# Optimization experiments

Hardware: AMD Instinct MI355X
Metric: run time of the kernel (lower is better)

## Reference

```python
import jax, jax.numpy as jnp
import numpy as np

N, T, D, H, NH, BS = 4, 4096, 512, 8, 4, 64
DH = D // H                 # head dim = 64
NB = T // BS                # n_buckets = 64
CS = NH * NB                # chunk_size = 256
L = NH * T                  # sorted sequence length per head


def setup_inputs() -> dict:
    key = jax.random.key(0)
    ks = jax.random.split(key, 4)
    x = jax.random.normal(ks[0], (N, T, D), jnp.float32)
    W_Q = jax.random.normal(ks[1], (D, D), jnp.float32) * (D ** -0.5)
    W_V = jax.random.normal(ks[2], (D, D), jnp.float32) * (D ** -0.5)
    b_Q = jnp.zeros((D,), jnp.float32)
    b_V = jnp.zeros((D,), jnp.float32)
    gamma = jnp.ones((D,), jnp.float32)
    beta = jnp.zeros((D,), jnp.float32)
    # per-head random rotations: (dim_head, num_hashes, n_buckets // 2)
    rotations = jax.random.normal(ks[3], (H, DH, NH, NB // 2), jnp.float32)
    return {"x": x, "W_Q": W_Q, "b_Q": b_Q, "W_V": W_V, "b_V": b_V,
            "gamma": gamma, "beta": beta, "rotations": rotations}


def _look_one_back(a):
    # concat each chunk with the previous chunk (wrap-around for chunk 0)
    extra = jnp.concatenate([a[:, -1:], a[:, :-1]], axis=1)
    return jnp.concatenate([a, extra], axis=2)


def _lsh_head(qk, v, rot):
    # qk, v: [N, T, DH]; rot: [DH, NH, NB//2]
    rotated = jnp.einsum('btf,fhi->bhti', qk, rot)               # [N,NH,T,NB//2]
    rotated = jnp.concatenate([rotated, -rotated], axis=-1)       # [N,NH,T,NB]
    buckets = jnp.argmax(rotated, axis=-1)                        # [N,NH,T]
    offsets = (jnp.arange(NH) * NB)[None, :, None]
    buckets = (buckets + offsets).reshape(N, L)                   # [N, NH*T]

    ticker = jnp.broadcast_to(jnp.arange(L)[None, :], (N, L))
    buckets_and_t = T * buckets + (ticker % T)                    # unique keys
    sticker = jnp.argsort(buckets_and_t, axis=-1)                 # sorted ticker ids
    undo_sort = jnp.argsort(sticker, axis=-1)
    st = sticker % T                                              # original positions

    sqk = jnp.take_along_axis(qk, st[..., None], axis=1)          # [N,L,DH]
    sv = jnp.take_along_axis(v, st[..., None], axis=1)

    bq_t = st.reshape(N, CS, -1)                                  # [N,CS,BS]
    bqk = sqk.reshape(N, CS, -1, DH)
    bv = sv.reshape(N, CS, -1, DH)
    bq = bqk
    bk = bqk / (jnp.linalg.norm(bqk, axis=-1, keepdims=True) + 1e-6)

    bk = _look_one_back(bk)                                       # [N,CS,2*BS,DH]
    bv = _look_one_back(bv)
    bkv_t = _look_one_back(bq_t)

    dots = jnp.einsum('bcie,bcje->bcij', bq, bk) * (DH ** -0.5)   # [N,CS,BS,2BS]

    # mask out pairs hashed to different buckets
    q_sb = jnp.take_along_axis(buckets, sticker, axis=1).reshape(N, CS, -1)
    kv_sb = _look_one_back(q_sb)
    dots = jnp.where(q_sb[:, :, :, None] != kv_sb[:, :, None, :], -1e9, dots)
    # down-weight self-attention (same position)
    dots = jnp.where(bq_t[:, :, :, None] == bkv_t[:, :, None, :], -1e-5, dots)

    lse = jax.nn.logsumexp(dots, axis=-1, keepdims=True)
    probs = jnp.exp(dots - lse)
    bo = jnp.einsum('bcij,bcje->bcie', probs, bv)                 # [N,CS,BS,DH]

    so = bo.reshape(N, L, DH)
    slog = lse.reshape(N, L)
    o = jnp.take_along_axis(so, undo_sort[..., None], axis=1)
    logits = jnp.take_along_axis(slog, undo_sort, axis=1)

    o = o.reshape(N, NH, T, DH)
    logits = logits.reshape(N, NH, T, 1)
    pw = jnp.exp(logits - jax.nn.logsumexp(logits, axis=1, keepdims=True))
    return jnp.sum(o * pw, axis=1)                                # [N,T,DH]


def reference(x, W_Q, b_Q, W_V, b_V, gamma, beta, rotations):
    Q = x @ W_Q + b_Q
    V = x @ W_V + b_V
    Qh = Q.reshape(N, T, H, DH).transpose(2, 0, 1, 3)             # [H,N,T,DH]
    Vh = V.reshape(N, T, H, DH).transpose(2, 0, 1, 3)
    outs = jax.vmap(_lsh_head)(Qh, Vh, rotations)                 # [H,N,T,DH]
    out = outs.transpose(1, 2, 0, 3).reshape(N, T, D)
    mu = out.mean(axis=-1, keepdims=True)
    var = out.var(axis=-1, keepdims=True)
    return gamma * (out - mu) / jnp.sqrt(var + 1e-3) + beta
```

## Files before the change

kernel.cpp:

```cpp
#include <hip/hip_runtime.h>
#include <hip/hip_bf16.h>

#define N_ 4
#define T_ 4096
#define D_ 512
#define H_ 8
#define DH_ 64
#define NH_ 4
#define NB_ 64
#define CS_ 256
#define L_ 16384

typedef unsigned short u16;
typedef unsigned int u32;
typedef __attribute__((ext_vector_type(8))) short short8;
typedef __attribute__((ext_vector_type(8))) _Float16 half8;
typedef __attribute__((ext_vector_type(4))) float f32x4;
typedef __attribute__((ext_vector_type(2))) float f32x2;

__device__ __forceinline__ u16 f2bf(float x){
    union { float f; u32 u; } c; c.f = x;
    u32 u = c.u;
    u32 r = (u + 0x7FFFu + ((u >> 16) & 1u)) >> 16;
    return (u16)r;
}
__device__ __forceinline__ float bf2f(u16 b){
    union { u32 u; float f; } c; c.u = ((u32)b) << 16;
    return c.f;
}
__device__ __forceinline__ u16 f2h(float x){
    _Float16 h = (_Float16)x;
    u16 r; __builtin_memcpy(&r, &h, 2); return r;
}

#define PK_LO(acc, a, b) \
    asm("v_pk_fma_f32 %0, %1, %2, %0 op_sel:[0,0,0] op_sel_hi:[0,1,1]" \
        : "+v"(acc) : "v"(a), "v"(b))
#define PK_HI(acc, a, b) \
    asm("v_pk_fma_f32 %0, %1, %2, %0 op_sel:[1,0,0] op_sel_hi:[1,1,1]" \
        : "+v"(acc) : "v"(a), "v"(b))

#define VSWZ(d) ((((d) >> 3) ^ ((d) & 7)))

__global__ __launch_bounds__(256) void k_decWv(const float* __restrict__ Wv,
        u16* __restrict__ wvt){
    __shared__ float tile[32][33];
    const int tid = threadIdx.x;
    const int kt = blockIdx.x * 32, nt = blockIdx.y * 32;
    const int tx = tid & 31, ty = tid >> 5;
    #pragma unroll
    for (int i = 0; i < 4; ++i)
        tile[ty + i * 8][tx] = Wv[(size_t)(kt + ty + i * 8) * 512 + nt + tx];
    __syncthreads();
    #pragma unroll
    for (int i = 0; i < 4; ++i){
        int n = ty + i * 8;
        wvt[(size_t)(nt + n) * 512 + kt + tx] = f2h(tile[tx][n]);
    }
}

__global__ __launch_bounds__(512, 4) void k_qv(const float* __restrict__ x,
        const float* __restrict__ Wq, const float* __restrict__ bq,
        const u16* __restrict__ wvt, const float* __restrict__ bv,
        float* __restrict__ Q, u16* __restrict__ Qbf, float* __restrict__ qinv,
        u16* __restrict__ Vbf){
    __shared__ __align__(16) char uLDS[33792];

    const int bid = blockIdx.x;
    const int role = (bid >> 8) & 1;
    const int id = ((bid >> 9) << 8) | (bid & 255);
    const int mb = (id & 127) * 128;
    const int nbi = id >> 7;
    const int nb = nbi * 128;
    const int tid = threadIdx.x;

    if (role == 0){
        typedef float (*pan_t)[16][132];
        pan_t sA = (pan_t)uLDS;
        pan_t sB = (pan_t)(uLDS + 16896);
        const int tx = tid & 31, ty = tid >> 5;
        f32x2 acc2[8][2];
        #pragma unroll
        for (int i = 0; i < 8; ++i){
            acc2[i][0] = (f32x2){0.f, 0.f};
            acc2[i][1] = (f32x2){0.f, 0.f};
        }
        const int mA = tid >> 2, kA = (tid & 3) * 4;
        const int kB = tid >> 5, cB = (tid & 31) * 4;
        const float* xp = &x[(size_t)(mb + mA) * 512 + kA];
        const float* wp = &Wq[(size_t)kB * 512 + nb + cB];
        float4 pa = *(const float4*)xp;
        float4 pb = *(const float4*)wp;

        for (int k0 = 0; k0 < 512; k0 += 16){
            const int p = (k0 >> 4) & 1;
            sA[p][kA + 0][mA] = pa.x; sA[p][kA + 1][mA] = pa.y;
            sA[p][kA + 2][mA] = pa.z; sA[p][kA + 3][mA] = pa.w;
            *(float4*)&sB[p][kB][cB] = pb;
            __syncthreads();
            if (k0 < 496){
                pa = *(const float4*)(xp + k0 + 16);
                pb = *(const float4*)(wp + (size_t)(k0 + 16) * 512);
            }
            #pragma unroll
            for (int kk = 0; kk < 16; ++kk){
                float4 va0 = *(const float4*)&sA[p][kk][ty * 8];
                float4 va1 = *(const float4*)&sA[p][kk][ty * 8 + 4];
                float4 vb  = *(const float4*)&sB[p][kk][tx * 4];
                f32x2 a2[4], b2[2];
                a2[0] = (f32x2){va0.x, va0.y}; a2[1] = (f32x2){va0.z, va0.w};
                a2[2] = (f32x2){va1.x, va1.y}; a2[3] = (f32x2){va1.z, va1.w};
                b2[0] = (f32x2){vb.x, vb.y};   b2[1] = (f32x2){vb.z, vb.w};
                #pragma unroll
                for (int i = 0; i < 8; ++i){
                    if (i & 1){
                        PK_HI(acc2[i][0], a2[i >> 1], b2[0]);
                        PK_HI(acc2[i][1], a2[i >> 1], b2[1]);
                    } else {
                        PK_LO(acc2[i][0], a2[i >> 1], b2[0]);
                        PK_LO(acc2[i][1], a2[i >> 1], b2[1]);
                    }
                }
            }
        }

        float4 vbq = *(const float4*)&bq[nb + tx * 4];
        const int h = nbi * 2 + (tx >> 4);
        const int d0 = (tx & 15) * 4;
        #pragma unroll
        for (int i = 0; i < 8; ++i){
            float o0 = acc2[i][0].x + vbq.x;
            float o1 = acc2[i][0].y + vbq.y;
            float o2 = acc2[i][1].x + vbq.z;
            float o3 = acc2[i][1].y + vbq.w;
            int m = mb + ty * 8 + i;
            int n = m >> 12, t = m & (T_ - 1);
            float4 q4; q4.x = o0; q4.y = o1; q4.z = o2; q4.w = o3;
            *(float4*)&Q[(size_t)m * 512 + nb + tx * 4] = q4;
            float ss = o0 * o0 + o1 * o1 + o2 * o2 + o3 * o3;
            #pragma unroll
            for (int s = 8; s >= 1; s >>= 1) ss += __shfl_xor(ss, s, 64);
            size_t rowb = (size_t)(h * N_ + n) * T_ + t;
            if ((tx & 15) == 0) qinv[rowb] = 1.f / (sqrtf(ss) + 1e-6f);
            ushort4 qb4;
            qb4.x = f2bf(o0); qb4.y = f2bf(o1); qb4.z = f2bf(o2); qb4.w = f2bf(o3);
            *(ushort4*)&Qbf[rowb * 64 + d0] = qb4;
        }
    } else {
        if (tid >= 256) return;
        u16* sA = (u16*)uLDS;
        u16* sB = (u16*)(uLDS + 10240);
        const int w = tid >> 6, lane = tid & 63;
        const int quad = lane >> 4, cc = lane & 15;
        const int wm = (w & 1) * 64, wn = (w >> 1) * 64;
        f32x4 acc[4][4];
        #pragma unroll
        for (int i = 0; i < 4; ++i)
            #pragma unroll
            for (int j = 0; j < 4; ++j) acc[i][j] = (f32x4){0.f, 0.f, 0.f, 0.f};

        for (int k0 = 0; k0 < 512; k0 += 32){
            #pragma unroll
            for (int i = 0; i < 2; ++i){
                int idx = i * 256 + tid;
                int m = idx >> 2, ks = idx & 3;
                const float* xs = &x[(size_t)(mb + m) * 512 + k0 + ks * 8];
                float4 f0 = *(const float4*)xs;
                float4 f1 = *(const float4*)(xs + 4);
                short8 s;
                s[0] = (short)f2h(f0.x); s[1] = (short)f2h(f0.y);
                s[2] = (short)f2h(f0.z); s[3] = (short)f2h(f0.w);
                s[4] = (short)f2h(f1.x); s[5] = (short)f2h(f1.y);
                s[6] = (short)f2h(f1.z); s[7] = (short)f2h(f1.w);
                *(short8*)&sA[m * 40 + ks * 8] = s;
                *(short8*)&sB[m * 40 + ks * 8] =
                    *(const short8*)&wvt[(size_t)(nb + m) * 512 + k0 + ks * 8];
            }
            __syncthreads();
            half8 a[4], b[4];
            #pragma unroll
            for (int i = 0; i < 4; ++i){
                a[i] = *(const half8*)&sA[(wm + i * 16 + cc) * 40 + quad * 8];
                b[i] = *(const half8*)&sB[(wn + i * 16 + cc) * 40 + quad * 8];
            }
            #pragma unroll
            for (int i = 0; i < 4; ++i)
                #pragma unroll
                for (int j = 0; j < 4; ++j)
                    acc[i][j] = __builtin_amdgcn_mfma_f32_16x16x32_f16(a[i], b[j], acc[i][j], 0, 0, 0);
            __syncthreads();
        }
        #pragma unroll
        for (int i = 0; i < 4; ++i)
            #pragma unroll
            for (int j = 0; j < 4; ++j){
                int c = nb + wn + j * 16 + cc;
                int hh = c >> 6, d = c & 63;
                float bi = bv[c];
                #pragma unroll
                for (int r = 0; r < 4; ++r){
                    int m = mb + wm + i * 16 + quad * 4 + r;
                    int n = m >> 12, t = m & (T_ - 1);
                    Vbf[((size_t)(hh * N_ + n) * T_ + t) * 64 + d] = f2bf(acc[i][j][r] + bi);
                }
            }
    }
}

__global__ __launch_bounds__(256) void k_rot(const float* __restrict__ Q,
        const float* __restrict__ rot, int* __restrict__ buckets){
    const int tb = blockIdx.x * 32;
    const int n = blockIdx.y, h = blockIdx.z;
    const int hn = h * N_ + n;
    __shared__ float Rs[64 * 128];
    __shared__ float Qs[32][64];
    const int tid = threadIdx.x;
    const float* rh = rot + (size_t)h * (64 * 128);
    for (int idx = tid; idx < 8192; idx += 256){
        int f = idx >> 7, rem = idx & 127, jj = rem >> 5, i2 = rem & 31;
        Rs[f * 128 + i2 * 4 + jj] = rh[idx];
    }
    for (int i = tid; i < 2048; i += 256){
        int t = i >> 6, f = i & 63;
        Qs[t][f] = Q[(size_t)(n * T_ + tb + t) * 512 + h * 64 + f];
    }
    __syncthreads();
    const int tx = tid & 31, tg = tid >> 5;
    f32x2 r2[4][2];
    #pragma unroll
    for (int tt = 0; tt < 4; ++tt){
        r2[tt][0] = (f32x2){0.f, 0.f};
        r2[tt][1] = (f32x2){0.f, 0.f};
    }
    for (int f = 0; f < 64; f += 2){
        f32x2 qf[4];
        #pragma unroll
        for (int tt = 0; tt < 4; ++tt)
            qf[tt] = *(const f32x2*)&Qs[tg * 4 + tt][f];
        float4 rv0 = *(const float4*)&Rs[f * 128 + tx * 4];
        float4 rv1 = *(const float4*)&Rs[(f + 1) * 128 + tx * 4];
        f32x2 b0[2], b1[2];
        b0[0] = (f32x2){rv0.x, rv0.y}; b0[1] = (f32x2){rv0.z, rv0.w};
        b1[0] = (f32x2){rv1.x, rv1.y}; b1[1] = (f32x2){rv1.z, rv1.w};
        #pragma unroll
        for (int tt = 0; tt < 4; ++tt){
            PK_LO(r2[tt][0], qf[tt], b0[0]);
            PK_LO(r2[tt][1], qf[tt], b0[1]);
            PK_HI(r2[tt][0], qf[tt], b1[0]);
            PK_HI(r2[tt][1], qf[tt], b1[1]);
        }
    }
    #pragma unroll
    for (int tt = 0; tt < 4; ++tt){
        #pragma unroll
        for (int jj = 0; jj < 4; ++jj){
            float rval = (jj < 2) ? r2[tt][0][jj] : r2[tt][1][jj - 2];
            float bv = rval; int bi = tx;
            float nv = -bv;
            if (nv > bv){ bv = nv; bi = 32 + tx; }
            #pragma unroll
            for (int m = 16; m >= 1; m >>= 1){
                float ov = __shfl_xor(bv, m, 32);
                int   oi = __shfl_xor(bi, m, 32);
                if (ov > bv || (ov == bv && oi < bi)){ bv = ov; bi = oi; }
            }
            if (tx == 0){
                int t = tb + tg * 4 + tt;
                buckets[(size_t)hn * L_ + jj * T_ + t] = bi + jj * 64;
            }
        }
    }
}

__global__ __launch_bounds__(256) void k_hist(const int* __restrict__ buckets,
        int* __restrict__ hist){
    const int tile = blockIdx.x, hn = blockIdx.y;
    const int tid = threadIdx.x;
    __shared__ int h[256];
    h[tid] = 0;
    __syncthreads();
    int b = buckets[(size_t)hn * L_ + tile * 256 + tid];
    atomicAdd(&h[b], 1);
    __syncthreads();
    hist[((size_t)hn * 64 + tile) * 256 + tid] = h[tid];
}

__global__ __launch_bounds__(256) void k_scan(int* __restrict__ hist,
        int* __restrict__ bucketStart){
    const int hn = blockIdx.x;
    const int b = threadIdx.x;
    int* hh = hist + (size_t)hn * 64 * 256;
    int run = 0;
    for (int tl = 0; tl < 64; ++tl){
        int v = hh[tl * 256 + b];
        hh[tl * 256 + b] = run;
        run += v;
    }
    __shared__ int s[256];
    s[b] = run;
    __syncthreads();
    for (int off = 1; off < 256; off <<= 1){
        int add = (b >= off) ? s[b - off] : 0;
        __syncthreads();
        s[b] += add;
        __syncthreads();
    }
    bucketStart[hn * 256 + b] = s[b] - run;
}

__global__ __launch_bounds__(256) void k_scatter(const int* __restrict__ buckets,
        const int* __restrict__ offs, const int* __restrict__ bucketStart,
        int* __restrict__ sticker){
    const int tile = blockIdx.x, hn = blockIdx.y;
    const int tid = threadIdx.x;
    __shared__ int sb[256];
    const int i = tile * 256 + tid;
    const int b = buckets[(size_t)hn * L_ + i];
    sb[tid] = b;
    __syncthreads();
    int rank = 0;
    #pragma unroll 8
    for (int j = 0; j < 256; ++j){
        int v = sb[j];
        rank += (j < tid && v == b) ? 1 : 0;
    }
    int pos = bucketStart[hn * 256 + b]
            + offs[((size_t)hn * 64 + tile) * 256 + b]
            + rank;
    sticker[(size_t)hn * L_ + pos] = i;
}

__global__ __launch_bounds__(256) void k_attn(const u16* __restrict__ Qbf,
        const u16* __restrict__ Vbf, const float* __restrict__ qinv,
        const int* __restrict__ buckets, const int* __restrict__ sticker,
        u16* __restrict__ o_hash, float* __restrict__ logit_hash){
    const int blk_c = blockIdx.x, n = blockIdx.y, h = blockIdx.z;
    const int hn = h * N_ + n;
    const int tid = threadIdx.x;
    const int w = tid >> 6, lane = tid & 63;
    const int quad = lane >> 4, cc = lane & 15;

    __shared__ __align__(16) u16 sQP[128 * 64];
    __shared__ __align__(16) u16 sVt[64 * 128];
    __shared__ int s_idx[128], s_buck[128], s_t[128];
    __shared__ float s_inv[128];
    __shared__ float s_lse[64];
    u16* const sQ = sQP;
    u16* const sP = sQP;

    if (tid < 128){
        int cprev = (blk_c + CS_ - 1) & (CS_ - 1);
        int pos = (tid < 64) ? blk_c * 64 + tid : cprev * 64 + (tid - 64);
        int idx = sticker[(size_t)hn * L_ + pos];
        s_idx[tid] = idx;
        s_buck[tid] = buckets[(size_t)hn * L_ + idx];
        int t = idx & (T_ - 1);
        s_t[tid] = t;
        s_inv[tid] = qinv[(size_t)hn * T_ + t] * 0.125f;
    }
    __syncthreads();

    const int r0 = tid >> 3, l8 = tid & 7;
    #pragma unroll
    for (int it = 0; it < 4; ++it){
        int r = it * 32 + r0;
        size_t gb = ((size_t)hn * T_ + s_t[r]) * 64 + l8 * 8;
        short8 qv = *(const short8*)&Qbf[gb];
        *(short8*)&sQ[r * 64 + ((l8 ^ (r & 7)) * 8)] = qv;
        short8 vv = *(const short8*)&Vbf[gb];
        #pragma unroll
        for (int i = 0; i < 8; ++i){
            int d = l8 * 8 + i;
            sVt[d * 128 + (((r >> 3) ^ VSWZ(d)) * 8) + (r & 7)] = (u16)vv[i];
        }
    }
    __syncthreads();

    f32x4 dacc[8];
    #pragma unroll
    for (int j = 0; j < 8; ++j) dacc[j] = (f32x4){0.f, 0.f, 0.f, 0.f};
    const int qrow = w * 16 + cc;
    #pragma unroll
    for (int kc = 0; kc < 2; ++kc){
        short8 afrag = *(const short8*)&sQ[qrow * 64 + (((kc * 4 + quad) ^ (cc & 7)) * 8)];
        #pragma unroll
        for (int kt = 0; kt < 8; ++kt){
            int krow = kt * 16 + cc;
            short8 bfrag = *(const short8*)&sQ[krow * 64 + (((kc * 4 + quad) ^ (cc & 7)) * 8)];
            dacc[kt] = __builtin_amdgcn_mfma_f32_16x16x32_bf16(afrag, bfrag, dacc[kt], 0, 0, 0);
        }
    }

    int bq[4], tq[4];
    #pragma unroll
    for (int r = 0; r < 4; ++r){
        int q = w * 16 + quad * 4 + r;
        bq[r] = s_buck[q]; tq[r] = s_t[q];
    }
    float mrow[4] = {-1e30f, -1e30f, -1e30f, -1e30f};
    #pragma unroll
    for (int kt = 0; kt < 8; ++kt){
        int kk = kt * 16 + cc;
        float inv = s_inv[kk];
        int bk = s_buck[kk], tk = s_t[kk];
        #pragma unroll
        for (int r = 0; r < 4; ++r){
            float d = dacc[kt][r] * inv;
            if (bk != bq[r]) d = -1e9f;
            if (tk == tq[r]) d = -1e-5f;
            dacc[kt][r] = d;
            mrow[r] = fmaxf(mrow[r], d);
        }
    }
    #pragma unroll
    for (int r = 0; r < 4; ++r)
        #pragma unroll
        for (int m = 8; m >= 1; m >>= 1)
            mrow[r] = fmaxf(mrow[r], __shfl_xor(mrow[r], m, 64));
    float srow[4] = {0.f, 0.f, 0.f, 0.f};
    #pragma unroll
    for (int kt = 0; kt < 8; ++kt)
        #pragma unroll
        for (int r = 0; r < 4; ++r){
            float e = __expf(dacc[kt][r] - mrow[r]);
            dacc[kt][r] = e;
            srow[r] += e;
        }
    #pragma unroll
    for (int r = 0; r < 4; ++r)
        #pragma unroll
        for (int m = 8; m >= 1; m >>= 1)
            srow[r] += __shfl_xor(srow[r], m, 64);
    float lse[4], pscale[4];
    #pragma unroll
    for (int r = 0; r < 4; ++r){
        lse[r] = mrow[r] + __logf(srow[r]);
        pscale[r] = 1.f / srow[r];
    }
    if (cc == 0){
        #pragma unroll
        for (int r = 0; r < 4; ++r) s_lse[w * 16 + quad * 4 + r] = lse[r];
    }

    __syncthreads();

    #pragma unroll
    for (int kt = 0; kt < 8; ++kt){
        int kk = kt * 16 + cc;
        #pragma unroll
        for (int r = 0; r < 4; ++r){
            int q = w * 16 + quad * 4 + r;
            sP[q * 128 + (((kk >> 3) ^ (q & 15)) * 8) + (kk & 7)] =
                f2bf(dacc[kt][r] * pscale[r]);
        }
    }
    __syncthreads();

    f32x4 oacc[4];
    #pragma unroll
    for (int j = 0; j < 4; ++j) oacc[j] = (f32x4){0.f, 0.f, 0.f, 0.f};
    #pragma unroll
    for (int kc = 0; kc < 4; ++kc){
        short8 afrag = *(const short8*)&sP[qrow * 128 + (((kc * 4 + quad) ^ cc) * 8)];
        #pragma unroll
        for (int nt = 0; nt < 4; ++nt){
            int d = nt * 16 + cc;
            short8 bfrag = *(const short8*)&sVt[d * 128 + (((kc * 4 + quad) ^ VSWZ(d)) * 8)];
            oacc[nt] = __builtin_amdgcn_mfma_f32_16x16x32_bf16(afrag, bfrag, oacc[nt], 0, 0, 0);
        }
    }

    #pragma unroll
    for (int r = 0; r < 4; ++r){
        int q = w * 16 + quad * 4 + r;
        int si = s_idx[q];
        int jj = si >> 12; int t = si & (T_ - 1);
        size_t base = ((size_t)(hn * NH_ + jj) * T_ + t) * 64;
        #pragma unroll
        for (int nt = 0; nt < 4; ++nt)
            o_hash[base + nt * 16 + cc] = f2bf(oacc[nt][r]);
    }
    if (tid < 64){
        int si = s_idx[tid]; int jj = si >> 12; int t = si & (T_ - 1);
        logit_hash[(size_t)(hn * NH_ + jj) * T_ + t] = s_lse[tid];
    }
}

__global__ __launch_bounds__(256) void k_comb(const u16* __restrict__ o_hash,
        const float* __restrict__ logit_hash, const float* __restrict__ gamma,
        const float* __restrict__ beta, float* __restrict__ out){
    const int t = blockIdx.x, n = blockIdx.y;
    const int tid = threadIdx.x;
    __shared__ float s_pw[32];
    __shared__ float s_x[512];
    __shared__ float s_red[8];
    __shared__ float s_mu, s_rs;
    if (tid < 32){
        int h = tid >> 2, j = tid & 3;
        s_pw[tid] = logit_hash[(size_t)((h * N_ + n) * NH_ + j) * T_ + t];
    }
    __syncthreads();
    if (tid < 8){
        int h = tid;
        float m = -1e30f;
        #pragma unroll
        for (int j = 0; j < 4; ++j) m = fmaxf(m, s_pw[h * 4 + j]);
        float l = 0.f;
        #pragma unroll
        for (int j = 0; j < 4; ++j) l += __expf(s_pw[h * 4 + j] - m);
        float ls = m + __logf(l);
        #pragma unroll
        for (int j = 0; j < 4; ++j) s_pw[h * 4 + j] = __expf(s_pw[h * 4 + j] - ls);
    }
    __syncthreads();
    float va[2];
    #pragma unroll
    for (int i = 0; i < 2; ++i){
        int cidx = tid + i * 256;
        int h = cidx >> 6, d = cidx & 63;
        size_t base = (size_t)((h * N_ + n) * NH_) * T_ * 64;
        float acc = 0.f;
        #pragma unroll
        for (int j = 0; j < 4; ++j)
            acc += s_pw[h * 4 + j] * bf2f(o_hash[base + ((size_t)j * T_ + t) * 64 + d]);
        s_x[cidx] = acc; va[i] = acc;
    }
    float s1 = va[0] + va[1];
    float s2 = va[0] * va[0] + va[1] * va[1];
    #pragma unroll
    for (int m = 32; m >= 1; m >>= 1){
        s1 += __shfl_xor(s1, m, 64);
        s2 += __shfl_xor(s2, m, 64);
    }
    const int lane = tid & 63, w = tid >> 6;
    if (lane == 0){ s_red[w] = s1; s_red[4 + w] = s2; }
    __syncthreads();
    if (tid == 0){
        float S1 = s_red[0] + s_red[1] + s_red[2] + s_red[3];
        float S2 = s_red[4] + s_red[5] + s_red[6] + s_red[7];
        float mu = S1 / 512.f;
        float var = S2 / 512.f - mu * mu;
        s_mu = mu; s_rs = 1.f / sqrtf(var + 1e-3f);
    }
    __syncthreads();
    #pragma unroll
    for (int i = 0; i < 2; ++i){
        int cidx = tid + i * 256;
        out[((size_t)(n * T_ + t)) * 512 + cidx] =
            gamma[cidx] * (s_x[cidx] - s_mu) * s_rs + beta[cidx];
    }
}

extern "C" void kernel_launch(void* const* d_in, const int* in_sizes, int n_in,
                              void* d_out, int out_size, void* d_ws, size_t ws_size,
                              hipStream_t stream){
    const float* x     = (const float*)d_in[0];
    const float* Wq    = (const float*)d_in[1];
    const float* bq    = (const float*)d_in[2];
    const float* Wv    = (const float*)d_in[3];
    const float* bv    = (const float*)d_in[4];
    const float* gamma = (const float*)d_in[5];
    const float* beta  = (const float*)d_in[6];
    const float* rot   = (const float*)d_in[7];
    char* ws = (char*)d_ws;
    float* Q        = (float*)(ws + 0);
    u16*   o_hash   = (u16*)  (ws + 0);
    u16*   Qbf      = (u16*)  (ws + 67108864);
    u16*   Vbf      = (u16*)  (ws + 83886080);
    float* qinv     = (float*)(ws + 100663296);
    int*   buckets  = (int*)  (ws + 101187584);
    int*   sticker  = (int*)  (ws + 103284736);
    float* logit    = (float*)(ws + 105381888);
    int*   hist     = (int*)  (ws + 107479040);
    int*   bstart   = (int*)  (ws + 109576192);
    u16*   wvt      = (u16*)  (ws + 109608960);

    hipLaunchKernelGGL(k_decWv,   dim3(16, 16),     dim3(256), 0, stream,
                       Wv, wvt);
    hipLaunchKernelGGL(k_qv,      dim3(1024),       dim3(512), 0, stream,
                       x, Wq, bq, wvt, bv, Q, Qbf, qinv, Vbf);
    hipLaunchKernelGGL(k_rot,     dim3(128, 4, 8),  dim3(256), 0, stream,
                       Q, rot, buckets);
    hipLaunchKernelGGL(k_hist,    dim3(64, 32),     dim3(256), 0, stream,
                       buckets, hist);
    hipLaunchKernelGGL(k_scan,    dim3(32),         dim3(256), 0, stream,
                       hist, bstart);
    hipLaunchKernelGGL(k_scatter, dim3(64, 32),     dim3(256), 0, stream,
                       buckets, hist, bstart, sticker);
    hipLaunchKernelGGL(k_attn,    dim3(256, 4, 8),  dim3(256), 0, stream,
                       Qbf, Vbf, qinv, buckets, sticker, o_hash, logit);
    hipLaunchKernelGGL(k_comb,    dim3(4096, 4),    dim3(256), 0, stream,
                       o_hash, logit, gamma, beta, (float*)d_out);
}
```

Baseline: 380.7 us.

## Interleave hash outputs per token, warp-per-token combine, amortize rotation loads, MFMA priority

Four changes land together. The o_hash and logit_hash layouts are reordered so the four hash rounds of each token sit next to each other, and k_comb now gives each wavefront one token, doing the softmax over rounds and the layer norm with shuffles instead of shared memory and block barriers. k_rot handles 64 tokens per block instead of 32, so each rotation-matrix load into LDS serves twice as many tokens, at the cost of fewer blocks. The attention MFMA loops are wrapped in s_setprio to raise wave priority while issuing matrix ops.

Result: slower. 397.5 us (+4.4%).

```diff
diff --git a/kernel.cpp b/kernel.cpp
--- a/kernel.cpp
+++ b/kernel.cpp
@@ -209,64 +209,66 @@
 
 __global__ __launch_bounds__(256) void k_rot(const float* __restrict__ Q,
         const float* __restrict__ rot, int* __restrict__ buckets){
-    const int tb = blockIdx.x * 32;
+    const int tb = blockIdx.x * 64;
     const int n = blockIdx.y, h = blockIdx.z;
     const int hn = h * N_ + n;
     __shared__ float Rs[64 * 128];
-    __shared__ float Qs[32][64];
+    __shared__ float Qs[64][64];
     const int tid = threadIdx.x;
     const float* rh = rot + (size_t)h * (64 * 128);
     for (int idx = tid; idx < 8192; idx += 256){
         int f = idx >> 7, rem = idx & 127, jj = rem >> 5, i2 = rem & 31;
         Rs[f * 128 + i2 * 4 + jj] = rh[idx];
     }
-    for (int i = tid; i < 2048; i += 256){
+    for (int i = tid; i < 4096; i += 256){
         int t = i >> 6, f = i & 63;
         Qs[t][f] = Q[(size_t)(n * T_ + tb + t) * 512 + h * 64 + f];
     }
     __syncthreads();
     const int tx = tid & 31, tg = tid >> 5;
-    f32x2 r2[4][2];
-    #pragma unroll
-    for (int tt = 0; tt < 4; ++tt){
-        r2[tt][0] = (f32x2){0.f, 0.f};
-        r2[tt][1] = (f32x2){0.f, 0.f};
-    }
-    for (int f = 0; f < 64; f += 2){
-        f32x2 qf[4];
-        #pragma unroll
-        for (int tt = 0; tt < 4; ++tt)
-            qf[tt] = *(const f32x2*)&Qs[tg * 4 + tt][f];
-        float4 rv0 = *(const float4*)&Rs[f * 128 + tx * 4];
-        float4 rv1 = *(const float4*)&Rs[(f + 1) * 128 + tx * 4];
-        f32x2 b0[2], b1[2];
-        b0[0] = (f32x2){rv0.x, rv0.y}; b0[1] = (f32x2){rv0.z, rv0.w};
-        b1[0] = (f32x2){rv1.x, rv1.y}; b1[1] = (f32x2){rv1.z, rv1.w};
+    for (int half = 0; half < 2; ++half){
+        f32x2 r2[4][2];
         #pragma unroll
         for (int tt = 0; tt < 4; ++tt){
-            PK_LO(r2[tt][0], qf[tt], b0[0]);
-            PK_LO(r2[tt][1], qf[tt], b0[1]);
-            PK_HI(r2[tt][0], qf[tt], b1[0]);
-            PK_HI(r2[tt][1], qf[tt], b1[1]);
-        }
-    }
-    #pragma unroll
-    for (int tt = 0; tt < 4; ++tt){
-        #pragma unroll
-        for (int jj = 0; jj < 4; ++jj){
-            float rval = (jj < 2) ? r2[tt][0][jj] : r2[tt][1][jj - 2];
-            float bv = rval; int bi = tx;
-            float nv = -bv;
-            if (nv > bv){ bv = nv; bi = 32 + tx; }
-            #pragma unroll
-            for (int m = 16; m >= 1; m >>= 1){
-                float ov = __shfl_xor(bv, m, 32);
-                int   oi = __shfl_xor(bi, m, 32);
-                if (ov > bv || (ov == bv && oi < bi)){ bv = ov; bi = oi; }
-            }
-            if (tx == 0){
-                int t = tb + tg * 4 + tt;
-                buckets[(size_t)hn * L_ + jj * T_ + t] = bi + jj * 64;
+            r2[tt][0] = (f32x2){0.f, 0.f};
+            r2[tt][1] = (f32x2){0.f, 0.f};
+        }
+        for (int f = 0; f < 64; f += 2){
+            f32x2 qf[4];
+            #pragma unroll
+            for (int tt = 0; tt < 4; ++tt)
+                qf[tt] = *(const f32x2*)&Qs[half * 32 + tg * 4 + tt][f];
+            float4 rv0 = *(const float4*)&Rs[f * 128 + tx * 4];
+            float4 rv1 = *(const float4*)&Rs[(f + 1) * 128 + tx * 4];
+            f32x2 b0[2], b1[2];
+            b0[0] = (f32x2){rv0.x, rv0.y}; b0[1] = (f32x2){rv0.z, rv0.w};
+            b1[0] = (f32x2){rv1.x, rv1.y}; b1[1] = (f32x2){rv1.z, rv1.w};
+            #pragma unroll
+            for (int tt = 0; tt < 4; ++tt){
+                PK_LO(r2[tt][0], qf[tt], b0[0]);
+                PK_LO(r2[tt][1], qf[tt], b0[1]);
+                PK_HI(r2[tt][0], qf[tt], b1[0]);
+                PK_HI(r2[tt][1], qf[tt], b1[1]);
+            }
+        }
+        #pragma unroll
+        for (int tt = 0; tt < 4; ++tt){
+            #pragma unroll
+            for (int jj = 0; jj < 4; ++jj){
+                float rval = (jj < 2) ? r2[tt][0][jj] : r2[tt][1][jj - 2];
+                float bv = rval; int bi = tx;
+                float nv = -bv;
+                if (nv > bv){ bv = nv; bi = 32 + tx; }
+                #pragma unroll
+                for (int m = 16; m >= 1; m >>= 1){
+                    float ov = __shfl_xor(bv, m, 32);
+                    int   oi = __shfl_xor(bi, m, 32);
+                    if (ov > bv || (ov == bv && oi < bi)){ bv = ov; bi = oi; }
+                }
+                if (tx == 0){
+                    int t = tb + half * 32 + tg * 4 + tt;
+                    buckets[(size_t)hn * L_ + jj * T_ + t] = bi + jj * 64;
+                }
             }
         }
     }
@@ -380,6 +382,7 @@
     #pragma unroll
     for (int j = 0; j < 8; ++j) dacc[j] = (f32x4){0.f, 0.f, 0.f, 0.f};
     const int qrow = w * 16 + cc;
+    __builtin_amdgcn_s_setprio(1);
     #pragma unroll
     for (int kc = 0; kc < 2; ++kc){
         short8 afrag = *(const short8*)&sQ[qrow * 64 + (((kc * 4 + quad) ^ (cc & 7)) * 8)];
@@ -390,6 +393,7 @@
             dacc[kt] = __builtin_amdgcn_mfma_f32_16x16x32_bf16(afrag, bfrag, dacc[kt], 0, 0, 0);
         }
     }
+    __builtin_amdgcn_s_setprio(0);
 
     int bq[4], tq[4];
     #pragma unroll
@@ -459,6 +463,7 @@
     f32x4 oacc[4];
     #pragma unroll
     for (int j = 0; j < 4; ++j) oacc[j] = (f32x4){0.f, 0.f, 0.f, 0.f};
+    __builtin_amdgcn_s_setprio(1);
     #pragma unroll
     for (int kc = 0; kc < 4; ++kc){
         short8 afrag = *(const short8*)&sP[qrow * 128 + (((kc * 4 + quad) ^ cc) * 8)];
@@ -469,85 +474,72 @@
             oacc[nt] = __builtin_amdgcn_mfma_f32_16x16x32_bf16(afrag, bfrag, oacc[nt], 0, 0, 0);
         }
     }
+    __builtin_amdgcn_s_setprio(0);
 
     #pragma unroll
     for (int r = 0; r < 4; ++r){
         int q = w * 16 + quad * 4 + r;
         int si = s_idx[q];
         int jj = si >> 12; int t = si & (T_ - 1);
-        size_t base = ((size_t)(hn * NH_ + jj) * T_ + t) * 64;
+        size_t base = (((size_t)hn * T_ + t) * NH_ + jj) * 64;
         #pragma unroll
         for (int nt = 0; nt < 4; ++nt)
             o_hash[base + nt * 16 + cc] = f2bf(oacc[nt][r]);
     }
     if (tid < 64){
         int si = s_idx[tid]; int jj = si >> 12; int t = si & (T_ - 1);
-        logit_hash[(size_t)(hn * NH_ + jj) * T_ + t] = s_lse[tid];
+        logit_hash[((size_t)hn * T_ + t) * NH_ + jj] = s_lse[tid];
     }
 }
 
 __global__ __launch_bounds__(256) void k_comb(const u16* __restrict__ o_hash,
         const float* __restrict__ logit_hash, const float* __restrict__ gamma,
         const float* __restrict__ beta, float* __restrict__ out){
-    const int t = blockIdx.x, n = blockIdx.y;
-    const int tid = threadIdx.x;
-    __shared__ float s_pw[32];
-    __shared__ float s_x[512];
-    __shared__ float s_red[8];
-    __shared__ float s_mu, s_rs;
-    if (tid < 32){
-        int h = tid >> 2, j = tid & 3;
-        s_pw[tid] = logit_hash[(size_t)((h * N_ + n) * NH_ + j) * T_ + t];
-    }
-    __syncthreads();
-    if (tid < 8){
-        int h = tid;
-        float m = -1e30f;
-        #pragma unroll
-        for (int j = 0; j < 4; ++j) m = fmaxf(m, s_pw[h * 4 + j]);
-        float l = 0.f;
-        #pragma unroll
-        for (int j = 0; j < 4; ++j) l += __expf(s_pw[h * 4 + j] - m);
-        float ls = m + __logf(l);
-        #pragma unroll
-        for (int j = 0; j < 4; ++j) s_pw[h * 4 + j] = __expf(s_pw[h * 4 + j] - ls);
-    }
-    __syncthreads();
-    float va[2];
-    #pragma unroll
-    for (int i = 0; i < 2; ++i){
-        int cidx = tid + i * 256;
-        int h = cidx >> 6, d = cidx & 63;
-        size_t base = (size_t)((h * N_ + n) * NH_) * T_ * 64;
-        float acc = 0.f;
-        #pragma unroll
-        for (int j = 0; j < 4; ++j)
-            acc += s_pw[h * 4 + j] * bf2f(o_hash[base + ((size_t)j * T_ + t) * 64 + d]);
-        s_x[cidx] = acc; va[i] = acc;
-    }
-    float s1 = va[0] + va[1];
-    float s2 = va[0] * va[0] + va[1] * va[1];
-    #pragma unroll
-    for (int m = 32; m >= 1; m >>= 1){
-        s1 += __shfl_xor(s1, m, 64);
-        s2 += __shfl_xor(s2, m, 64);
-    }
-    const int lane = tid & 63, w = tid >> 6;
-    if (lane == 0){ s_red[w] = s1; s_red[4 + w] = s2; }
-    __syncthreads();
-    if (tid == 0){
-        float S1 = s_red[0] + s_red[1] + s_red[2] + s_red[3];
-        float S2 = s_red[4] + s_red[5] + s_red[6] + s_red[7];
-        float mu = S1 / 512.f;
-        float var = S2 / 512.f - mu * mu;
-        s_mu = mu; s_rs = 1.f / sqrtf(var + 1e-3f);
-    }
-    __syncthreads();
-    #pragma unroll
-    for (int i = 0; i < 2; ++i){
-        int cidx = tid + i * 256;
-        out[((size_t)(n * T_ + t)) * 512 + cidx] =
-            gamma[cidx] * (s_x[cidx] - s_mu) * s_rs + beta[cidx];
+    const int n = blockIdx.y;
+    const int tid = threadIdx.x;
+    const int w = tid >> 6, lane = tid & 63;
+    const int t = blockIdx.x * 4 + w;
+
+    float pwv = 0.f;
+    if (lane < 32){
+        int h = lane >> 2, j = lane & 3;
+        pwv = logit_hash[((size_t)(h * N_ + n) * T_ + t) * NH_ + j];
+    }
+    float m = fmaxf(pwv, __shfl_xor(pwv, 1, 64));
+    m = fmaxf(m, __shfl_xor(m, 2, 64));
+    float e = __expf(pwv - m);
+    float l = e + __shfl_xor(e, 1, 64);
+    l += __shfl_xor(l, 2, 64);
+    float wgt = __expf(pwv - (m + __logf(l)));
+
+    float acc[8];
+    #pragma unroll
+    for (int h = 0; h < 8; ++h){
+        size_t base = ((size_t)(h * N_ + n) * T_ + t) * (NH_ * 64);
+        float a = 0.f;
+        #pragma unroll
+        for (int j = 0; j < 4; ++j){
+            float wj = __shfl(wgt, h * 4 + j, 64);
+            a += wj * bf2f(o_hash[base + j * 64 + lane]);
+        }
+        acc[h] = a;
+    }
+    float s1 = 0.f, s2 = 0.f;
+    #pragma unroll
+    for (int h = 0; h < 8; ++h){ s1 += acc[h]; s2 += acc[h] * acc[h]; }
+    #pragma unroll
+    for (int ms = 32; ms >= 1; ms >>= 1){
+        s1 += __shfl_xor(s1, ms, 64);
+        s2 += __shfl_xor(s2, ms, 64);
+    }
+    float mu = s1 / 512.f;
+    float var = s2 / 512.f - mu * mu;
+    float rs = 1.f / sqrtf(var + 1e-3f);
+    #pragma unroll
+    for (int h = 0; h < 8; ++h){
+        int c = h * 64 + lane;
+        out[((size_t)(n * T_ + t)) * 512 + c] =
+            gamma[c] * (acc[h] - mu) * rs + beta[c];
     }
 }
 
@@ -579,7 +571,7 @@
                        Wv, wvt);
     hipLaunchKernelGGL(k_qv,      dim3(1024),       dim3(512), 0, stream,
                        x, Wq, bq, wvt, bv, Q, Qbf, qinv, Vbf);
-    hipLaunchKernelGGL(k_rot,     dim3(128, 4, 8),  dim3(256), 0, stream,
+    hipLaunchKernelGGL(k_rot,     dim3(64, 4, 8),   dim3(256), 0, stream,
                        Q, rot, buckets);
     hipLaunchKernelGGL(k_hist,    dim3(64, 32),     dim3(256), 0, stream,
                        buckets, hist);
@@ -589,6 +581,6 @@
                        buckets, hist, bstart, sticker);
     hipLaunchKernelGGL(k_attn,    dim3(256, 4, 8),  dim3(256), 0, stream,
                        Qbf, Vbf, qinv, buckets, sticker, o_hash, logit);
-    hipLaunchKernelGGL(k_comb,    dim3(4096, 4),    dim3(256), 0, stream,
+    hipLaunchKernelGGL(k_comb,    dim3(1024, 4),    dim3(256), 0, stream,
                        o_hash, logit, gamma, beta, (float*)d_out);
 }
```
